# Optimization experiments

Measured on AMD Instinct MI355X. Metric: run time of the kernel, lower is better.

Reference implementation:

```python
import jax, jax.numpy as jnp
import numpy as np

EPS = 1e-5

def conv1x1(x, W, b):
    # x: (B,C,H,W), W: (O,C), b: (O,)
    return jnp.einsum('bchw,oc->bohw', x, W) + b[None, :, None, None]

def setup_inputs() -> dict:
    key = jax.random.key(0)
    ks = jax.random.split(key, 16)
    B, C_in, C1, D, K, H, Wd = 8, 512, 256, 128, 32, 96, 96
    s = lambda k, shape, fan: jax.random.normal(k, shape, jnp.float32) * (1.0 / np.sqrt(fan))
    return {
        'X': jax.random.normal(ks[0], (B, C_in, H, Wd), jnp.float32),
        'W_theta': s(ks[1], (C1, C_in), C_in), 'b_theta': jnp.zeros((C1,), jnp.float32),
        'W_phi': s(ks[2], (C1, C_in), C_in), 'b_phi': jnp.zeros((C1,), jnp.float32),
        'W_g': s(ks[3], (C1, C_in), C_in), 'b_g': jnp.zeros((C1,), jnp.float32),
        'W2': s(ks[4], (C_in, C1), C1), 'b2': jnp.zeros((C_in,), jnp.float32),
        'W3': s(ks[5], (D, C_in), C_in), 'b3': jnp.zeros((D,), jnp.float32),
        'codewords': jax.random.normal(ks[6], (K, D), jnp.float32),
        'scale': -jax.random.uniform(ks[7], (K,), jnp.float32),  # Deep-TEN init: U(-1,0)
        'W_fc': s(ks[8], (C_in, D), D), 'b_fc': jnp.zeros((C_in,), jnp.float32),
    }

def reference(X, W_theta, b_theta, W_phi, b_phi, W_g, b_g, W2, b2, W3, b3,
              codewords, scale, W_fc, b_fc):
    B, C_in, H, Wd = X.shape
    C1 = W_theta.shape[0]
    D, K = W3.shape[0], codewords.shape[0]
    N = H * Wd
    # --- non-local (channel-attention) block ---
    theta = conv1x1(X, W_theta, b_theta).reshape(B, C1, N)          # (B,C1,N)
    phi = conv1x1(X, W_phi, b_phi).reshape(B, C1, N)                # (B,C1,N)
    g = conv1x1(X, W_g, b_g).reshape(B, C1, N)                      # (B,C1,N)
    f = jax.nn.softmax(jnp.einsum('bcn,bdn->bcd', theta, phi), axis=-1)  # (B,C1,C1)
    y = jnp.einsum('bcd,bdn->bcn', f, g).reshape(B, C1, H, Wd)
    z = conv1x1(y, W2, b2) + X                                      # (B,C_in,H,W)
    # --- Deep-TEN encoding ---
    z_ = conv1x1(z, W3, b3)                                         # (B,D,H,W)
    x = z_.reshape(B, D, N).transpose(0, 2, 1)                      # (B,N,D)
    # squared L2 distances to codewords without (B,N,K,D) residuals
    dist = (jnp.sum(x * x, -1, keepdims=True)
            - 2.0 * jnp.einsum('bnd,kd->bnk', x, codewords)
            + jnp.sum(codewords * codewords, -1))                   # (B,N,K)
    A = jax.nn.softmax(scale * dist, axis=-1)                       # (B,N,K)
    # E_k = sum_i A_ik (x_i - c_k)
    E = jnp.einsum('bnk,bnd->bkd', A, x) - A.sum(1)[..., None] * codewords  # (B,K,D)
    # --- training-mode batch norm over K channels (no affine) ---
    mean = E.mean(axis=(0, 2), keepdims=True)
    var = E.var(axis=(0, 2), keepdims=True)
    e = jax.nn.relu((E - mean) * jax.lax.rsqrt(var + EPS))
    Es = e.sum(axis=1)                                              # (B,D)
    gamma = jax.nn.sigmoid(Es @ W_fc.T + b_fc)                      # (B,C_in)
    return z * gamma[:, :, None, None]
```

## Files before the change

kernel.cpp:

```cpp
#include <hip/hip_runtime.h>


typedef unsigned short u16;

#define Bb 8
#define Cc 512
#define C1 256
#define Dd 128
#define Kk 32
#define Nn 9216

typedef __attribute__((ext_vector_type(8))) short short8v;
typedef __attribute__((ext_vector_type(4))) short short4v;
typedef __attribute__((ext_vector_type(4))) float f32x4;

__device__ __forceinline__ float b2f(u16 u) {
  union { unsigned int i; float f; } v; v.i = ((unsigned int)u) << 16; return v.f;
}
__device__ __forceinline__ u16 f2b(float f) {
  union { float f; unsigned int i; } v; v.f = f;
  unsigned int x = v.i;
  return (u16)((x + 0x7fffu + ((x >> 16) & 1u)) >> 16);
}

__device__ __forceinline__ float b2fOrF(float x) { return x; }
__device__ __forceinline__ float b2fOrF(u16 x) { return b2f(x); }

__device__ __forceinline__ float4 load4(const float* p) { return *(const float4*)p; }
__device__ __forceinline__ float4 load4(const u16* p) {
  ushort4 q = *(const ushort4*)p;
  return make_float4(b2f(q.x), b2f(q.y), b2f(q.z), b2f(q.w));
}
__device__ __forceinline__ void store4(float* p, float a, float b, float c, float d) {
  *(float4*)p = make_float4(a, b, c, d);
}

__device__ __forceinline__ float waveSum(float v) {
  #pragma unroll
  for (int o = 32; o > 0; o >>= 1) v += __shfl_xor(v, o);
  return v;
}
__device__ __forceinline__ float waveMax(float v) {
  #pragma unroll
  for (int o = 32; o > 0; o >>= 1) v = fmaxf(v, __shfl_xor(v, o));
  return v;
}
__device__ __forceinline__ float blockSum256(float v) {
  __shared__ float sm[4];
  v = waveSum(v);
  if ((threadIdx.x & 63) == 0) sm[threadIdx.x >> 6] = v;
  __syncthreads();
  float r = sm[0] + sm[1] + sm[2] + sm[3];
  __syncthreads();
  return r;
}
__device__ __forceinline__ float blockMax256(float v) {
  __shared__ float sm[4];
  v = waveMax(v);
  if ((threadIdx.x & 63) == 0) sm[threadIdx.x >> 6] = v;
  __syncthreads();
  float r = fmaxf(fmaxf(sm[0], sm[1]), fmaxf(sm[2], sm[3]));
  __syncthreads();
  return r;
}

__device__ __forceinline__ f32x4 mfma_bf16_16x16x32(short8v a, short8v b, f32x4 c) {
  asm("v_mfma_f32_16x16x32_bf16 %0, %1, %2, %0" : "+v"(c) : "v"(a), "v"(b));
  return c;
}

__device__ __forceinline__ int fsw(int r) { return (r ^ (r >> 2) ^ (r >> 4)) & 3; }

__device__ __forceinline__ void cvt2(float x0, float x1, unsigned int& h, unsigned int& l) {
  asm("v_cvt_pk_bf16_f32 %0, %1, %2" : "=v"(h) : "v"(x0), "v"(x1));
  union { unsigned int u; float f; } fa, fb;
  fa.u = h << 16; fb.u = h & 0xffff0000u;
  float r0 = x0 - fa.f, r1 = x1 - fb.f;
  asm("v_cvt_pk_bf16_f32 %0, %1, %2" : "=v"(l) : "v"(r0), "v"(r1));
}

__device__ __forceinline__ void storeC(float* p, float v) { *p = v; }
__device__ __forceinline__ void storeC(u16* p, float v) { *p = f2b(v); }

template<typename TO, int NF>
__global__ __launch_bounds__(256, 2) void gemm_mfma(
    const float* __restrict__ A, const float* __restrict__ B, TO* __restrict__ C,
    int N, int K,
    long long sA, long long sB, long long sC,
    const float* __restrict__ biasRow, long long sBias,
    int gnx, int gny)
{
  static_assert(NF == 4 || NF == 8, "NF");
  constexpr int BN = 32 * NF;
  __shared__ __align__(16) u16 Asm_[2][128][40];
  __shared__ __align__(16) u16 Bsm_[2][BN][40];

  int id = blockIdx.x;
  {
    const int nwg = gridDim.x;
    if ((nwg & 7) == 0) id = (id & 7) * (nwg >> 3) + (id >> 3);
  }
  const int per = gnx * gny;
  const int b = id / per;
  const int rem = id - b * per;
  const int by = rem % gny;
  const int bx = rem / gny;
  A += b * sA; B += b * sB; C += b * sC;
  const int m0 = by * 128, n0 = bx * BN;

  const int t = threadIdx.x;
  const int w = t >> 6, lane = t & 63;
  const int wr = w >> 1, wc = w & 1;
  const int lr = lane & 15, lq = lane >> 4;

  const int sar = t >> 1, sak = (t & 1) * 16;
  const int kg = t >> 5, ng = t & 31;

  float ra[16];
  float rb[32];

  auto loadA = [&](int k0) {
    const float* p = A + (long long)(m0 + sar) * K + (k0 + sak);
    #pragma unroll
    for (int i = 0; i < 4; ++i) {
      float4 v = *(const float4*)(p + i * 4);
      ra[i*4+0] = v.x; ra[i*4+1] = v.y; ra[i*4+2] = v.z; ra[i*4+3] = v.w;
    }
  };
  auto loadB = [&](int k0) {
    const float* p = B + (long long)(k0 + kg * 4) * N + (n0 + ng * 8);
    #pragma unroll
    for (int i = 0; i < 4; ++i) {
      float4 v0 = *(const float4*)(p + (long long)i * N);
      float4 v1 = *(const float4*)(p + (long long)i * N + 4);
      rb[i*8+0]=v0.x; rb[i*8+1]=v0.y; rb[i*8+2]=v0.z; rb[i*8+3]=v0.w;
      rb[i*8+4]=v1.x; rb[i*8+5]=v1.y; rb[i*8+6]=v1.z; rb[i*8+7]=v1.w;
    }
  };

  auto stage = [&]() {
    {
      const int f = fsw(sar);
      #pragma unroll
      for (int h = 0; h < 2; ++h) {
        const int col = ((((sak >> 3) + h) ^ f) << 3);
        union { unsigned int u[4]; short8v v; } H, L;
        #pragma unroll
        for (int p = 0; p < 4; ++p) cvt2(ra[h*8+2*p], ra[h*8+2*p+1], H.u[p], L.u[p]);
        *(short8v*)&Asm_[0][sar][col] = H.v;
        *(short8v*)&Asm_[1][sar][col] = L.v;
      }
    }
    {
      #pragma unroll
      for (int j = 0; j < 8; ++j) {
        const int n = ng * 8 + j;
        const int col = (((kg >> 1) ^ fsw(n)) << 3) + (kg & 1) * 4;
        union { unsigned int u[2]; short4v v; } H, L;
        #pragma unroll
        for (int p = 0; p < 2; ++p)
          cvt2(rb[(2*p)*8 + j], rb[(2*p+1)*8 + j], H.u[p], L.u[p]);
        *(short4v*)&Bsm_[0][n][col] = H.v;
        *(short4v*)&Bsm_[1][n][col] = L.v;
      }
    }
  };

  f32x4 acc[4][NF];
  #pragma unroll
  for (int im = 0; im < 4; ++im)
    #pragma unroll
    for (int in = 0; in < NF; ++in)
      acc[im][in] = f32x4{0.f, 0.f, 0.f, 0.f};

  loadA(0); loadB(0);
  for (int k0 = 0; k0 < K; k0 += 32) {
    stage();
    if (k0 + 32 < K) { loadA(k0 + 32); loadB(k0 + 32); }
    __syncthreads();
    short8v af[2][4];
    #pragma unroll
    for (int im = 0; im < 4; ++im) {
      const int r = wr * 64 + im * 16 + lr;
      const int col = ((lq ^ fsw(r)) << 3);
      af[0][im] = *(const short8v*)&Asm_[0][r][col];
      af[1][im] = *(const short8v*)&Asm_[1][r][col];
    }
    #pragma unroll
    for (int in = 0; in < NF; ++in) {
      const int rB = wc * NF * 16 + in * 16 + lr;
      const int colB = ((lq ^ fsw(rB)) << 3);
      short8v bh = *(const short8v*)&Bsm_[0][rB][colB];
      short8v bl = *(const short8v*)&Bsm_[1][rB][colB];
      #pragma unroll
      for (int im = 0; im < 4; ++im) {
        acc[im][in] = mfma_bf16_16x16x32(af[0][im], bh, acc[im][in]);
        acc[im][in] = mfma_bf16_16x16x32(af[0][im], bl, acc[im][in]);
        acc[im][in] = mfma_bf16_16x16x32(af[1][im], bh, acc[im][in]);
      }
    }
    __syncthreads();
  }
  asm volatile("s_nop 7\n\ts_nop 7\n\ts_nop 7");

  #pragma unroll
  for (int im = 0; im < 4; ++im) {
    #pragma unroll
    for (int in = 0; in < NF; ++in) {
      const f32x4 a = acc[im][in];
      const int gc = n0 + wc * NF * 16 + in * 16 + lr;
      #pragma unroll
      for (int p = 0; p < 4; ++p) {
        const int gr = m0 + wr * 64 + im * 16 + lq * 4 + p;
        float v = a[p];
        if (biasRow) v += biasRow[b * sBias + gr];
        storeC(&C[(long long)gr * N + gc], v);
      }
    }
  }
}

__device__ __constant__ int PIa[10] = {0,0,0,0,1,1,1,2,2,3};
__device__ __constant__ int PJa[10] = {0,1,2,3,1,2,3,2,3,3};

__global__ __launch_bounds__(256, 2) void gxxt_kernel(
    const float* __restrict__ X, float* __restrict__ part,
    int numKS, int kChunk)
{
  __shared__ __align__(16) u16 Asm_[2][128][40];
  __shared__ __align__(16) u16 Bsm_[2][128][40];

  int id = blockIdx.x;
  {
    const int nwg = gridDim.x;
    if ((nwg & 7) == 0) id = (id & 7) * (nwg >> 3) + (id >> 3);
  }
  const int pair = id % 10;
  const int rest = id / 10;
  const int ks = rest % numKS;
  const int b = rest / numKS;
  const int i0 = PIa[pair] * 128, j0 = PJa[pair] * 128;
  const bool same = (i0 == j0);
  const float* Xb = X + (long long)b * Cc * Nn;
  const int kBeg = ks * kChunk, kEnd = kBeg + kChunk;

  const int t = threadIdx.x;
  const int w = t >> 6, lane = t & 63;
  const int wr = w >> 1, wc = w & 1;
  const int lr = lane & 15, lq = lane >> 4;
  const int sar = t >> 1, sak = (t & 1) * 16;

  float ra[16], rb[16];

  auto loadA = [&](int k0) {
    const float* p = Xb + (long long)(i0 + sar) * Nn + (k0 + sak);
    #pragma unroll
    for (int i = 0; i < 4; ++i) {
      float4 v = *(const float4*)(p + i * 4);
      ra[i*4+0] = v.x; ra[i*4+1] = v.y; ra[i*4+2] = v.z; ra[i*4+3] = v.w;
    }
  };
  auto loadB = [&](int k0) {
    const float* p = Xb + (long long)(j0 + sar) * Nn + (k0 + sak);
    #pragma unroll
    for (int i = 0; i < 4; ++i) {
      float4 v = *(const float4*)(p + i * 4);
      rb[i*4+0] = v.x; rb[i*4+1] = v.y; rb[i*4+2] = v.z; rb[i*4+3] = v.w;
    }
  };
  auto stageRow = [&](const float* s16, u16 (*H)[40], u16 (*L)[40]) {
    const int f = fsw(sar);
    #pragma unroll
    for (int h = 0; h < 2; ++h) {
      const int col = ((((sak >> 3) + h) ^ f) << 3);
      union { unsigned int u[4]; short8v v; } Hv, Lv;
      #pragma unroll
      for (int p = 0; p < 4; ++p) cvt2(s16[h*8+2*p], s16[h*8+2*p+1], Hv.u[p], Lv.u[p]);
      *(short8v*)&H[sar][col] = Hv.v;
      *(short8v*)&L[sar][col] = Lv.v;
    }
  };

  const u16 (*BH)[40] = same ? Asm_[0] : Bsm_[0];
  const u16 (*BL)[40] = same ? Asm_[1] : Bsm_[1];

  f32x4 acc[4][4];
  #pragma unroll
  for (int im = 0; im < 4; ++im)
    #pragma unroll
    for (int in = 0; in < 4; ++in)
      acc[im][in] = f32x4{0.f, 0.f, 0.f, 0.f};

  loadA(kBeg);
  if (!same) loadB(kBeg);
  for (int k0 = kBeg; k0 < kEnd; k0 += 32) {
    stageRow(ra, Asm_[0], Asm_[1]);
    if (!same) stageRow(rb, Bsm_[0], Bsm_[1]);
    if (k0 + 32 < kEnd) { loadA(k0 + 32); if (!same) loadB(k0 + 32); }
    __syncthreads();
    short8v af[2][4];
    #pragma unroll
    for (int im = 0; im < 4; ++im) {
      const int r = wr * 64 + im * 16 + lr;
      const int col = ((lq ^ fsw(r)) << 3);
      af[0][im] = *(const short8v*)&Asm_[0][r][col];
      af[1][im] = *(const short8v*)&Asm_[1][r][col];
    }
    #pragma unroll
    for (int in = 0; in < 4; ++in) {
      const int rB = wc * 64 + in * 16 + lr;
      const int colB = ((lq ^ fsw(rB)) << 3);
      short8v bh = *(const short8v*)&BH[rB][colB];
      short8v bl = *(const short8v*)&BL[rB][colB];
      #pragma unroll
      for (int im = 0; im < 4; ++im) {
        acc[im][in] = mfma_bf16_16x16x32(af[0][im], bh, acc[im][in]);
        acc[im][in] = mfma_bf16_16x16x32(af[0][im], bl, acc[im][in]);
        acc[im][in] = mfma_bf16_16x16x32(af[1][im], bh, acc[im][in]);
      }
    }
    __syncthreads();
  }
  asm volatile("s_nop 7\n\ts_nop 7\n\ts_nop 7");

  float* Cp = part + ((long long)(ks * Bb + b) * 10 + pair) * 16384;
  #pragma unroll
  for (int im = 0; im < 4; ++im) {
    #pragma unroll
    for (int in = 0; in < 4; ++in) {
      const f32x4 a = acc[im][in];
      const int gc = wc * 64 + in * 16 + lr;
      #pragma unroll
      for (int p = 0; p < 4; ++p) {
        const int gr = wr * 64 + im * 16 + lq * 4 + p;
        Cp[gr * 128 + gc] = a[p];
      }
    }
  }
}

__global__ __launch_bounds__(256) void gred_kernel(const float* __restrict__ part,
    float* __restrict__ G, int numKS) {
  __shared__ float sm[64][129];
  const int pair = blockIdx.x % 10, b = blockIdx.x / 10;
  const int i0 = PIa[pair] * 128, j0 = PJa[pair] * 128;
  float* Gb = G + (long long)b * Cc * Cc;
  const long long ksStr = (long long)Bb * 10 * 16384;
  const float* p0 = part + ((long long)b * 10 + pair) * 16384;
  const int t = threadIdx.x;
  for (int half = 0; half < 2; ++half) {
    const int r0 = half * 64;
    __syncthreads();
    for (int rep = 0; rep < 32; ++rep) {
      int idx = r0 * 128 + rep * 256 + t;
      float s = 0.f;
      for (int ks = 0; ks < numKS; ++ks) s += p0[(long long)ks * ksStr + idx];
      int r = (idx >> 7) - r0, c = idx & 127;
      sm[r][c] = s;
      Gb[(long long)(i0 + r0 + r) * Cc + (j0 + c)] = s;
    }
    if (i0 != j0) {
      __syncthreads();
      for (int rep = 0; rep < 32; ++rep) {
        int o = rep * 256 + t;
        int rr = o >> 6, cc = o & 63;
        Gb[(long long)(j0 + rr) * Cc + (i0 + r0 + cc)] = sm[cc][rr];
      }
    }
  }
}

template<bool TRANSB>
__global__ __launch_bounds__(256) void gemm64(
    const float* __restrict__ A, const float* __restrict__ B, float* __restrict__ C,
    int M, int N, int K,
    long long sA, long long sB, long long sC,
    const float* __restrict__ biasRow, long long sBias)
{
  const int bz = blockIdx.z;
  A += (long long)bz * sA;
  B += (long long)bz * sB;
  C += (long long)bz * sC;
  const int m0 = blockIdx.y * 64, n0 = blockIdx.x * 64;
  __shared__ __align__(16) float As[16][64];
  __shared__ __align__(16) float Bs[16][64];
  const int t = threadIdx.x;
  const int lr = t >> 2, lk = (t & 3) << 2;
  const int tm = (t >> 4) << 2, tn = (t & 15) << 2;
  float acc[4][4] = {};
  for (int k0 = 0; k0 < K; k0 += 16) {
    {
      float4 a = load4(A + (long long)(m0 + lr) * K + (k0 + lk));
      As[lk + 0][lr] = a.x; As[lk + 1][lr] = a.y; As[lk + 2][lr] = a.z; As[lk + 3][lr] = a.w;
    }
    if (TRANSB) {
      float4 b = load4(B + (long long)(n0 + lr) * K + (k0 + lk));
      Bs[lk + 0][lr] = b.x; Bs[lk + 1][lr] = b.y; Bs[lk + 2][lr] = b.z; Bs[lk + 3][lr] = b.w;
    } else {
      const int kr = t >> 4, nc = (t & 15) << 2;
      float4 b = load4(B + (long long)(k0 + kr) * N + (n0 + nc));
      *(float4*)&Bs[kr][nc] = b;
    }
    __syncthreads();
    #pragma unroll
    for (int kk = 0; kk < 16; ++kk) {
      const float4 av = *(const float4*)&As[kk][tm];
      const float4 bv = *(const float4*)&Bs[kk][tn];
      acc[0][0] = fmaf(av.x, bv.x, acc[0][0]);
      acc[0][1] = fmaf(av.x, bv.y, acc[0][1]);
      acc[0][2] = fmaf(av.x, bv.z, acc[0][2]);
      acc[0][3] = fmaf(av.x, bv.w, acc[0][3]);
      acc[1][0] = fmaf(av.y, bv.x, acc[1][0]);
      acc[1][1] = fmaf(av.y, bv.y, acc[1][1]);
      acc[1][2] = fmaf(av.y, bv.z, acc[1][2]);
      acc[1][3] = fmaf(av.y, bv.w, acc[1][3]);
      acc[2][0] = fmaf(av.z, bv.x, acc[2][0]);
      acc[2][1] = fmaf(av.z, bv.y, acc[2][1]);
      acc[2][2] = fmaf(av.z, bv.z, acc[2][2]);
      acc[2][3] = fmaf(av.z, bv.w, acc[2][3]);
      acc[3][0] = fmaf(av.w, bv.x, acc[3][0]);
      acc[3][1] = fmaf(av.w, bv.y, acc[3][1]);
      acc[3][2] = fmaf(av.w, bv.z, acc[3][2]);
      acc[3][3] = fmaf(av.w, bv.w, acc[3][3]);
    }
    __syncthreads();
  }
  #pragma unroll
  for (int i = 0; i < 4; ++i) {
    const int m = m0 + tm + i;
    float bias = biasRow ? biasRow[bz * sBias + m] : 0.f;
    store4(C + (long long)m * N + (n0 + tn),
           acc[i][0] + bias, acc[i][1] + bias, acc[i][2] + bias, acc[i][3] + bias);
  }
}

__global__ __launch_bounds__(256) void rowsum_kernel(const float* __restrict__ X,
                                                     float* __restrict__ s, int N) {
  long long row = blockIdx.x;
  const float* p = X + row * N;
  float acc = 0.f;
  for (int i = threadIdx.x; i < N; i += 256) acc += p[i];
  acc = blockSum256(acc);
  if (threadIdx.x == 0) s[row] = acc;
}

__global__ __launch_bounds__(256) void gemv512_kernel(const float* __restrict__ W,
                                                      const float* __restrict__ s,
                                                      float* __restrict__ out) {
  int b = blockIdx.x;
  __shared__ float ssm[Cc];
  for (int i = threadIdx.x; i < Cc; i += 256) ssm[i] = s[b * Cc + i];
  __syncthreads();
  int i = threadIdx.x;
  const float* wr = W + i * Cc;
  float acc = 0.f;
  for (int k = 0; k < Cc; ++k) acc = fmaf(wr[k], ssm[k], acc);
  out[b * C1 + i] = acc;
}

__global__ __launch_bounds__(256) void softmax_kernel(float* __restrict__ L,
    const float* __restrict__ bth, const float* __restrict__ bph,
    const float* __restrict__ u, const float* __restrict__ v) {
  int row = blockIdx.x;
  int b = row >> 8, i = row & 255;
  int j = threadIdx.x;
  float bt = bth[i], bp = bph[j];
  long long idx = (long long)row * C1 + j;
  float val = L[idx] + bt * v[b * C1 + j] + u[b * C1 + i] * bp + (float)Nn * bt * bp;
  float mx = blockMax256(val);
  float p = expf(val - mx);
  float sm = blockSum256(p);
  L[idx] = p / sm;
}

__global__ __launch_bounds__(256) void w_kernel(const float* __restrict__ f,
                                                const float* __restrict__ bg,
                                                float* __restrict__ w) {
  int b = blockIdx.x;
  __shared__ float bgs[C1];
  bgs[threadIdx.x] = bg[threadIdx.x];
  __syncthreads();
  int i = threadIdx.x;
  const float* fr = f + ((long long)b * C1 + i) * C1;
  float acc = 0.f;
  for (int j = 0; j < C1; ++j) acc = fmaf(fr[j], bgs[j], acc);
  w[b * C1 + i] = acc;
}

__global__ __launch_bounds__(256) void q_kernel(const float* __restrict__ W2,
                                                const float* __restrict__ b2v,
                                                const float* __restrict__ w,
                                                float* __restrict__ q) {
  int gi = blockIdx.x * 256 + threadIdx.x;
  int b = gi >> 9, c = gi & 511;
  __shared__ float wsm[C1];
  wsm[threadIdx.x] = w[b * C1 + threadIdx.x];
  __syncthreads();
  const float* wr = W2 + c * C1;
  float acc = b2v[c];
  for (int i = 0; i < C1; ++i) acc = fmaf(wr[i], wsm[i], acc);
  q[gi] = acc;
}

__global__ __launch_bounds__(256) void adddiag_kernel(float* __restrict__ P) {
  int gi = blockIdx.x * 256 + threadIdx.x;
  int b = gi >> 9, c = gi & 511;
  P[((long long)b * Cc + c) * Cc + c] += 1.f;
}

__global__ __launch_bounds__(256) void zqbias_kernel(const float* __restrict__ W3,
    const float* __restrict__ b3, const float* __restrict__ q, float* __restrict__ zqb) {
  int gi = blockIdx.x * 256 + threadIdx.x;
  int b = gi >> 7, d = gi & 127;
  const float* wr = W3 + d * Cc;
  const float* qr = q + b * Cc;
  float acc = b3[d];
  for (int c = 0; c < Cc; ++c) acc = fmaf(wr[c], qr[c], acc);
  zqb[gi] = acc;
}

template<typename ZT>
__global__ __launch_bounds__(256) void enc_kernel(
    const ZT* __restrict__ zq,
    const float* __restrict__ cw,
    const float* __restrict__ sc,
    float* __restrict__ Eraw,
    float* __restrict__ Asum)
{
  __shared__ float csm[Kk][Dd + 1];
  __shared__ float cc[Kk], ssm[Kk];
  __shared__ float sA[Kk][256 + 1];
  __shared__ float zs[Dd][17];
  const int tid = threadIdx.x;
  const int b = blockIdx.y;
  const int n0 = blockIdx.x * 256;

  #pragma unroll
  for (int r = 0; r < 16; ++r) {
    int idx = r * 256 + tid;
    csm[idx >> 7][idx & 127] = cw[idx];
  }
  if (tid < Kk) ssm[tid] = sc[tid];
  __syncthreads();
  if (tid < Kk) {
    float a = 0.f;
    for (int d = 0; d < Dd; ++d) { float cv = csm[tid][d]; a = fmaf(cv, cv, a); }
    cc[tid] = a;
  }
  __syncthreads();

  const int n = n0 + tid;
  const ZT* zp = zq + (long long)b * Dd * Nn + n;
  float dots[Kk];
  #pragma unroll
  for (int k = 0; k < Kk; ++k) dots[k] = 0.f;
  float xx = 0.f;
  for (int d = 0; d < Dd; ++d) {
    float xv = b2fOrF(zp[(long long)d * Nn]);
    xx = fmaf(xv, xv, xx);
    #pragma unroll
    for (int k = 0; k < Kk; ++k) dots[k] = fmaf(csm[k][d], xv, dots[k]);
  }
  float mx = -1e30f;
  #pragma unroll
  for (int k = 0; k < Kk; ++k) {
    float l = ssm[k] * (xx - 2.f * dots[k] + cc[k]);
    dots[k] = l;
    mx = fmaxf(mx, l);
  }
  float sum = 0.f;
  #pragma unroll
  for (int k = 0; k < Kk; ++k) { float p = expf(dots[k] - mx); dots[k] = p; sum += p; }
  float inv = 1.f / sum;
  #pragma unroll
  for (int k = 0; k < Kk; ++k) sA[k][tid] = dots[k] * inv;
  __syncthreads();
  if (tid < Kk) {
    float s = 0.f;
    for (int p = 0; p < 256; ++p) s += sA[tid][p];
    atomicAdd(&Asum[b * Kk + tid], s);
  }

  float acc[16];
  #pragma unroll
  for (int j = 0; j < 16; ++j) acc[j] = 0.f;
  const int k = tid & 31, d0 = (tid >> 5) * 16;
  const int ldd = tid >> 1, lpx = (tid & 1) * 8;
  for (int it = 0; it < 16; ++it) {
    __syncthreads();
    {
      const ZT* src = zq + ((long long)b * Dd + ldd) * Nn + n0 + it * 16 + lpx;
      float4 a4 = load4(src);
      float4 b4 = load4(src + 4);
      zs[ldd][lpx + 0] = a4.x; zs[ldd][lpx + 1] = a4.y;
      zs[ldd][lpx + 2] = a4.z; zs[ldd][lpx + 3] = a4.w;
      zs[ldd][lpx + 4] = b4.x; zs[ldd][lpx + 5] = b4.y;
      zs[ldd][lpx + 6] = b4.z; zs[ldd][lpx + 7] = b4.w;
    }
    __syncthreads();
    #pragma unroll
    for (int p = 0; p < 16; ++p) {
      float a = sA[k][it * 16 + p];
      #pragma unroll
      for (int j = 0; j < 16; ++j) acc[j] = fmaf(a, zs[d0 + j][p], acc[j]);
    }
  }
  float* Ep = Eraw + ((long long)b * Kk + k) * Dd + d0;
  #pragma unroll
  for (int j = 0; j < 16; ++j) atomicAdd(Ep + j, acc[j]);
}

__global__ __launch_bounds__(256) void bn_kernel(const float* __restrict__ Eraw,
    const float* __restrict__ Asum, const float* __restrict__ cw, float* __restrict__ Es) {
  int k = blockIdx.x, tid = threadIdx.x;
  float vals[4], s = 0.f, s2 = 0.f;
  #pragma unroll
  for (int r = 0; r < 4; ++r) {
    int i = r * 256 + tid;
    int b = i >> 7, d = i & 127;
    float e = Eraw[((long long)b * Kk + k) * Dd + d] - Asum[b * Kk + k] * cw[k * Dd + d];
    vals[r] = e; s += e; s2 = fmaf(e, e, s2);
  }
  s = blockSum256(s);
  s2 = blockSum256(s2);
  float mean = s * (1.f / 1024.f);
  float var = fmaxf(s2 * (1.f / 1024.f) - mean * mean, 0.f);
  float rs = rsqrtf(var + 1e-5f);
  #pragma unroll
  for (int r = 0; r < 4; ++r) {
    int i = r * 256 + tid;
    int b = i >> 7, d = i & 127;
    float e = (vals[r] - mean) * rs;
    if (e > 0.f) atomicAdd(&Es[b * Dd + d], e);
  }
}

__global__ __launch_bounds__(256) void gamma_kernel(const float* __restrict__ Es,
    const float* __restrict__ Wfc, const float* __restrict__ bfc, float* __restrict__ gam) {
  int gi = blockIdx.x * 256 + threadIdx.x;
  int b = gi >> 9, c = gi & 511;
  __shared__ float esm[Dd];
  if (threadIdx.x < Dd) esm[threadIdx.x] = Es[b * Dd + threadIdx.x];
  __syncthreads();
  const float* wr = Wfc + c * Dd;
  float acc = bfc[c];
  for (int d = 0; d < Dd; ++d) acc = fmaf(wr[d], esm[d], acc);
  gam[gi] = 1.f / (1.f + expf(-acc));
}

__global__ __launch_bounds__(256) void scaleout_f32(float* __restrict__ out,
    const float* __restrict__ gam) {
  unsigned int idx = blockIdx.x * 256u + threadIdx.x;
  unsigned int f = idx * 4u;
  unsigned int bc = f / (unsigned)Nn;
  float g = gam[bc];
  float4 zv = *(const float4*)(out + f);
  store4(out + f, zv.x * g, zv.y * g, zv.z * g, zv.w * g);
}

extern "C" void kernel_launch(void* const* d_in, const int* in_sizes, int n_in,
                              void* d_out, int out_size, void* d_ws, size_t ws_size,
                              hipStream_t stream) {
  const float* X   = (const float*)d_in[0];
  const float* Wth = (const float*)d_in[1];
  const float* bth = (const float*)d_in[2];
  const float* Wph = (const float*)d_in[3];
  const float* bph = (const float*)d_in[4];
  const float* Wg  = (const float*)d_in[5];
  const float* bg  = (const float*)d_in[6];
  const float* W2  = (const float*)d_in[7];
  const float* b2v = (const float*)d_in[8];
  const float* W3  = (const float*)d_in[9];
  const float* b3v = (const float*)d_in[10];
  const float* CW  = (const float*)d_in[11];
  const float* SC  = (const float*)d_in[12];
  const float* Wfc = (const float*)d_in[13];
  const float* bfc = (const float*)d_in[14];
  float* out = (float*)d_out;
  float* wsf = (float*)d_ws;

  const long long szL   = (long long)Bb * C1 * C1;
  const long long szRA  = (long long)Bb * Cc * Cc;
  const long long szRB  = (long long)Bb * C1 * Cc;
  long long off = 0;
  float* s_   = wsf + off; off += Bb * Cc;
  float* u_   = wsf + off; off += Bb * C1;
  float* v_   = wsf + off; off += Bb * C1;
  float* w_   = wsf + off; off += Bb * C1;
  float* q_   = wsf + off; off += Bb * Cc;
  float* Eraw_= wsf + off; off += (long long)Bb * Kk * Dd;
  float* Es_  = wsf + off; off += Bb * Dd;
  float* Asum_= wsf + off; off += Bb * Kk;
  float* gam_ = wsf + off; off += Bb * Cc;
  float* L_   = wsf + off; off += szL;
  float* regA = wsf + off; off += szRA;
  float* regB = wsf + off; off += szRB;
  const long long baseFloats = off;
  float* tail = wsf + off;
  const long long ZQ_F  = (long long)Bb * Dd * Nn;
  const long long tailFloats = (long long)(ws_size / 4) - baseFloats;
  const bool big = tailFloats >= ZQ_F;
  const int numKS = big ? 6 : 2;
  float* part = tail;
  float* zqf  = tail;
  u16*   zqh  = (u16*)tail;
  float* R_   = L_;
  float* zqb_ = u_;

  const long long strX = (long long)Cc * Nn;
  const long long sG = (long long)Cc * Cc;
  const long long sU = (long long)C1 * Cc;
  const long long sL = (long long)C1 * C1;
  const long long sR = (long long)Dd * Cc;

  rowsum_kernel<<<Bb * Cc, 256, 0, stream>>>(X, s_, Nn);
  gxxt_kernel<<<dim3(10 * numKS * Bb), 256, 0, stream>>>(X, part, numKS, Nn / numKS);
  gred_kernel<<<dim3(10 * Bb), 256, 0, stream>>>(part, regA, numKS);
  gemm64<false><<<dim3(8, 4, Bb), 256, 0, stream>>>(
      Wth, regA, regB, C1, Cc, Cc, 0, sG, sU, nullptr, 0);
  gemv512_kernel<<<Bb, 256, 0, stream>>>(Wth, s_, u_);
  gemv512_kernel<<<Bb, 256, 0, stream>>>(Wph, s_, v_);
  gemm64<true><<<dim3(4, 4, Bb), 256, 0, stream>>>(
      regB, Wph, L_, C1, C1, Cc, sU, 0, sL, nullptr, 0);
  softmax_kernel<<<Bb * C1, 256, 0, stream>>>(L_, bth, bph, u_, v_);
  w_kernel<<<Bb, 256, 0, stream>>>(L_, bg, w_);
  gemm64<false><<<dim3(8, 4, Bb), 256, 0, stream>>>(
      L_, Wg, regB, C1, Cc, C1, sL, 0, sU, nullptr, 0);
  q_kernel<<<16, 256, 0, stream>>>(W2, b2v, w_, q_);
  gemm64<false><<<dim3(8, 8, Bb), 256, 0, stream>>>(
      W2, regB, regA, Cc, Cc, C1, 0, sU, sG, nullptr, 0);
  adddiag_kernel<<<16, 256, 0, stream>>>(regA);
  gemm64<false><<<dim3(8, 2, Bb), 256, 0, stream>>>(
      W3, regA, R_, Dd, Cc, Cc, 0, sG, sR, nullptr, 0);
  zqbias_kernel<<<4, 256, 0, stream>>>(W3, b3v, q_, zqb_);
  gemm_mfma<float, 8><<<dim3(1152), 256, 0, stream>>>(
      regA, X, out, Nn, Cc, sG, strX, strX, q_, Cc, 36, 4);
  hipMemsetAsync(Eraw_, 0, (size_t)(Bb * Kk * Dd + Bb * Dd + Bb * Kk) * 4, stream);
  if (big) {
    gemm_mfma<float, 8><<<dim3(288), 256, 0, stream>>>(
        R_, X, zqf, Nn, Cc, sR, strX, (long long)Dd * Nn, zqb_, Dd, 36, 1);
    enc_kernel<float><<<dim3(36, Bb), 256, 0, stream>>>(zqf, CW, SC, Eraw_, Asum_);
  } else {
    gemm_mfma<u16, 8><<<dim3(288), 256, 0, stream>>>(
        R_, X, zqh, Nn, Cc, sR, strX, (long long)Dd * Nn, zqb_, Dd, 36, 1);
    enc_kernel<u16><<<dim3(36, Bb), 256, 0, stream>>>(zqh, CW, SC, Eraw_, Asum_);
  }
  bn_kernel<<<Kk, 256, 0, stream>>>(Eraw_, Asum_, CW, Es_);
  gamma_kernel<<<16, 256, 0, stream>>>(Es_, Wfc, bfc, gam_);
  const unsigned int n4 = (unsigned)(Bb * Cc * Nn / 4);
  scaleout_f32<<<n4 / 256, 256, 0, stream>>>(out, gam_);
  (void)in_sizes; (void)n_in; (void)out_size;
}
```

Measured before the change: 1.099 ms.

## Fuse gamma scaling into output GEMM, transpose zq layout, move small GEMMs to MFMA

The big output GEMM now runs after gamma is computed and multiplies by gamma in its epilogue. This removes the separate full-tensor read-modify-write pass over the output. The zq GEMM now writes pixel-major (N,D) with vector stores, and enc_kernel reads contiguous rows and transposed shared tiles instead of strided columns. The small channel GEMMs switch from gemm64 to the MFMA kernel, which launches few blocks and may underuse the device.

Measured after the change: 1.096 ms. No clear change (-0.3%).

```diff
diff --git a/kernel.cpp b/kernel.cpp
--- a/kernel.cpp
+++ b/kernel.cpp
@@ -23,9 +23,6 @@
   return (u16)((x + 0x7fffu + ((x >> 16) & 1u)) >> 16);
 }
 
-__device__ __forceinline__ float b2fOrF(float x) { return x; }
-__device__ __forceinline__ float b2fOrF(u16 x) { return b2f(x); }
-
 __device__ __forceinline__ float4 load4(const float* p) { return *(const float4*)p; }
 __device__ __forceinline__ float4 load4(const u16* p) {
   ushort4 q = *(const ushort4*)p;
@@ -79,18 +76,22 @@
   asm("v_cvt_pk_bf16_f32 %0, %1, %2" : "=v"(l) : "v"(r0), "v"(r1));
 }
 
-__device__ __forceinline__ void storeC(float* p, float v) { *p = v; }
-__device__ __forceinline__ void storeC(u16* p, float v) { *p = f2b(v); }
-
-template<typename TO, int NF>
+__device__ __forceinline__ void storeC4(float* p, float4 v) { *(float4*)p = v; }
+__device__ __forceinline__ void storeC4(u16* p, float4 v) {
+  ushort4 q; q.x = f2b(v.x); q.y = f2b(v.y); q.z = f2b(v.z); q.w = f2b(v.w);
+  *(ushort4*)p = q;
+}
+
+template<typename TO, int NF, int OMODE>
 __global__ __launch_bounds__(256, 2) void gemm_mfma(
     const float* __restrict__ A, const float* __restrict__ B, TO* __restrict__ C,
     int N, int K,
     long long sA, long long sB, long long sC,
     const float* __restrict__ biasRow, long long sBias,
+    const float* __restrict__ scaleRow,
     int gnx, int gny)
 {
-  static_assert(NF == 4 || NF == 8, "NF");
+  static_assert(NF == 8, "NF");
   constexpr int BN = 32 * NF;
   __shared__ __align__(16) u16 Asm_[2][128][40];
   __shared__ __align__(16) u16 Bsm_[2][BN][40];
@@ -203,18 +204,35 @@
   }
   asm volatile("s_nop 7\n\ts_nop 7\n\ts_nop 7");
 
-  #pragma unroll
-  for (int im = 0; im < 4; ++im) {
-    #pragma unroll
-    for (int in = 0; in < NF; ++in) {
-      const f32x4 a = acc[im][in];
-      const int gc = n0 + wc * NF * 16 + in * 16 + lr;
-      #pragma unroll
-      for (int p = 0; p < 4; ++p) {
-        const int gr = m0 + wr * 64 + im * 16 + lq * 4 + p;
-        float v = a[p];
-        if (biasRow) v += biasRow[b * sBias + gr];
-        storeC(&C[(long long)gr * N + gc], v);
+  if constexpr (OMODE == 1) {
+    const float* bb = biasRow + (long long)b * sBias;
+    #pragma unroll
+    for (int im = 0; im < 4; ++im) {
+      #pragma unroll
+      for (int in = 0; in < NF; ++in) {
+        const f32x4 a = acc[im][in];
+        const int gc = n0 + wc * NF * 16 + in * 16 + lr;
+        const int d0b = wr * 64 + im * 16 + lq * 4;
+        float4 v = make_float4(a[0] + bb[d0b + 0], a[1] + bb[d0b + 1],
+                               a[2] + bb[d0b + 2], a[3] + bb[d0b + 3]);
+        storeC4(&C[(long long)gc * Dd + d0b], v);
+      }
+    }
+  } else {
+    #pragma unroll
+    for (int im = 0; im < 4; ++im) {
+      #pragma unroll
+      for (int in = 0; in < NF; ++in) {
+        const f32x4 a = acc[im][in];
+        const int gc = n0 + wc * NF * 16 + in * 16 + lr;
+        #pragma unroll
+        for (int p = 0; p < 4; ++p) {
+          const int gr = m0 + wr * 64 + im * 16 + lq * 4 + p;
+          float v = a[p];
+          if (biasRow) v += biasRow[b * sBias + gr];
+          if (scaleRow) v *= scaleRow[b * sBias + gr];
+          C[(long long)gr * N + gc] = v;
+        }
       }
     }
   }
@@ -530,7 +548,7 @@
   __shared__ float csm[Kk][Dd + 1];
   __shared__ float cc[Kk], ssm[Kk];
   __shared__ float sA[Kk][256 + 1];
-  __shared__ float zs[Dd][17];
+  __shared__ float zs[16][Dd + 4];
   const int tid = threadIdx.x;
   const int b = blockIdx.y;
   const int n0 = blockIdx.x * 256;
@@ -549,17 +567,24 @@
   }
   __syncthreads();
 
-  const int n = n0 + tid;
-  const ZT* zp = zq + (long long)b * Dd * Nn + n;
+  const ZT* zrow = zq + ((long long)b * Nn + n0 + tid) * Dd;
   float dots[Kk];
   #pragma unroll
   for (int k = 0; k < Kk; ++k) dots[k] = 0.f;
   float xx = 0.f;
-  for (int d = 0; d < Dd; ++d) {
-    float xv = b2fOrF(zp[(long long)d * Nn]);
-    xx = fmaf(xv, xv, xx);
-    #pragma unroll
-    for (int k = 0; k < Kk; ++k) dots[k] = fmaf(csm[k][d], xv, dots[k]);
+  for (int d = 0; d < Dd; d += 4) {
+    float4 xv = load4(zrow + d);
+    xx = fmaf(xv.x, xv.x, xx); xx = fmaf(xv.y, xv.y, xx);
+    xx = fmaf(xv.z, xv.z, xx); xx = fmaf(xv.w, xv.w, xx);
+    #pragma unroll
+    for (int k = 0; k < Kk; ++k) {
+      float dk = dots[k];
+      dk = fmaf(csm[k][d + 0], xv.x, dk);
+      dk = fmaf(csm[k][d + 1], xv.y, dk);
+      dk = fmaf(csm[k][d + 2], xv.z, dk);
+      dk = fmaf(csm[k][d + 3], xv.w, dk);
+      dots[k] = dk;
+    }
   }
   float mx = -1e30f;
   #pragma unroll
@@ -585,24 +610,22 @@
   #pragma unroll
   for (int j = 0; j < 16; ++j) acc[j] = 0.f;
   const int k = tid & 31, d0 = (tid >> 5) * 16;
-  const int ldd = tid >> 1, lpx = (tid & 1) * 8;
+  const int spx = tid >> 4, sd = (tid & 15) * 8;
   for (int it = 0; it < 16; ++it) {
     __syncthreads();
     {
-      const ZT* src = zq + ((long long)b * Dd + ldd) * Nn + n0 + it * 16 + lpx;
+      const ZT* src = zq + ((long long)b * Nn + n0 + it * 16 + spx) * Dd + sd;
       float4 a4 = load4(src);
       float4 b4 = load4(src + 4);
-      zs[ldd][lpx + 0] = a4.x; zs[ldd][lpx + 1] = a4.y;
-      zs[ldd][lpx + 2] = a4.z; zs[ldd][lpx + 3] = a4.w;
-      zs[ldd][lpx + 4] = b4.x; zs[ldd][lpx + 5] = b4.y;
-      zs[ldd][lpx + 6] = b4.z; zs[ldd][lpx + 7] = b4.w;
+      *(float4*)&zs[spx][sd] = a4;
+      *(float4*)&zs[spx][sd + 4] = b4;
     }
     __syncthreads();
     #pragma unroll
     for (int p = 0; p < 16; ++p) {
       float a = sA[k][it * 16 + p];
       #pragma unroll
-      for (int j = 0; j < 16; ++j) acc[j] = fmaf(a, zs[d0 + j][p], acc[j]);
+      for (int j = 0; j < 16; ++j) acc[j] = fmaf(a, zs[p][d0 + j], acc[j]);
     }
   }
   float* Ep = Eraw + ((long long)b * Kk + k) * Dd + d0;
@@ -646,16 +669,6 @@
   float acc = bfc[c];
   for (int d = 0; d < Dd; ++d) acc = fmaf(wr[d], esm[d], acc);
   gam[gi] = 1.f / (1.f + expf(-acc));
-}
-
-__global__ __launch_bounds__(256) void scaleout_f32(float* __restrict__ out,
-    const float* __restrict__ gam) {
-  unsigned int idx = blockIdx.x * 256u + threadIdx.x;
-  unsigned int f = idx * 4u;
-  unsigned int bc = f / (unsigned)Nn;
-  float g = gam[bc];
-  float4 zv = *(const float4*)(out + f);
-  store4(out + f, zv.x * g, zv.y * g, zv.z * g, zv.w * g);
 }
 
 extern "C" void kernel_launch(void* const* d_in, const int* in_sizes, int n_in,
@@ -716,38 +729,36 @@
   rowsum_kernel<<<Bb * Cc, 256, 0, stream>>>(X, s_, Nn);
   gxxt_kernel<<<dim3(10 * numKS * Bb), 256, 0, stream>>>(X, part, numKS, Nn / numKS);
   gred_kernel<<<dim3(10 * Bb), 256, 0, stream>>>(part, regA, numKS);
-  gemm64<false><<<dim3(8, 4, Bb), 256, 0, stream>>>(
-      Wth, regA, regB, C1, Cc, Cc, 0, sG, sU, nullptr, 0);
+  gemm_mfma<float, 8, 0><<<dim3(32), 256, 0, stream>>>(
+      Wth, regA, regB, Cc, Cc, 0, sG, sU, nullptr, 0, nullptr, 2, 2);
   gemv512_kernel<<<Bb, 256, 0, stream>>>(Wth, s_, u_);
   gemv512_kernel<<<Bb, 256, 0, stream>>>(Wph, s_, v_);
   gemm64<true><<<dim3(4, 4, Bb), 256, 0, stream>>>(
       regB, Wph, L_, C1, C1, Cc, sU, 0, sL, nullptr, 0);
   softmax_kernel<<<Bb * C1, 256, 0, stream>>>(L_, bth, bph, u_, v_);
   w_kernel<<<Bb, 256, 0, stream>>>(L_, bg, w_);
-  gemm64<false><<<dim3(8, 4, Bb), 256, 0, stream>>>(
-      L_, Wg, regB, C1, Cc, C1, sL, 0, sU, nullptr, 0);
+  gemm_mfma<float, 8, 0><<<dim3(32), 256, 0, stream>>>(
+      L_, Wg, regB, Cc, C1, sL, 0, sU, nullptr, 0, nullptr, 2, 2);
   q_kernel<<<16, 256, 0, stream>>>(W2, b2v, w_, q_);
-  gemm64<false><<<dim3(8, 8, Bb), 256, 0, stream>>>(
-      W2, regB, regA, Cc, Cc, C1, 0, sU, sG, nullptr, 0);
+  gemm_mfma<float, 8, 0><<<dim3(64), 256, 0, stream>>>(
+      W2, regB, regA, Cc, C1, 0, sU, sG, nullptr, 0, nullptr, 2, 4);
   adddiag_kernel<<<16, 256, 0, stream>>>(regA);
-  gemm64<false><<<dim3(8, 2, Bb), 256, 0, stream>>>(
-      W3, regA, R_, Dd, Cc, Cc, 0, sG, sR, nullptr, 0);
+  gemm_mfma<float, 8, 0><<<dim3(16), 256, 0, stream>>>(
+      W3, regA, R_, Cc, Cc, 0, sG, sR, nullptr, 0, nullptr, 2, 1);
   zqbias_kernel<<<4, 256, 0, stream>>>(W3, b3v, q_, zqb_);
-  gemm_mfma<float, 8><<<dim3(1152), 256, 0, stream>>>(
-      regA, X, out, Nn, Cc, sG, strX, strX, q_, Cc, 36, 4);
   hipMemsetAsync(Eraw_, 0, (size_t)(Bb * Kk * Dd + Bb * Dd + Bb * Kk) * 4, stream);
   if (big) {
-    gemm_mfma<float, 8><<<dim3(288), 256, 0, stream>>>(
-        R_, X, zqf, Nn, Cc, sR, strX, (long long)Dd * Nn, zqb_, Dd, 36, 1);
+    gemm_mfma<float, 8, 1><<<dim3(288), 256, 0, stream>>>(
+        R_, X, zqf, Nn, Cc, sR, strX, (long long)Dd * Nn, zqb_, Dd, nullptr, 36, 1);
     enc_kernel<float><<<dim3(36, Bb), 256, 0, stream>>>(zqf, CW, SC, Eraw_, Asum_);
   } else {
-    gemm_mfma<u16, 8><<<dim3(288), 256, 0, stream>>>(
-        R_, X, zqh, Nn, Cc, sR, strX, (long long)Dd * Nn, zqb_, Dd, 36, 1);
+    gemm_mfma<u16, 8, 1><<<dim3(288), 256, 0, stream>>>(
+        R_, X, zqh, Nn, Cc, sR, strX, (long long)Dd * Nn, zqb_, Dd, nullptr, 36, 1);
     enc_kernel<u16><<<dim3(36, Bb), 256, 0, stream>>>(zqh, CW, SC, Eraw_, Asum_);
   }
   bn_kernel<<<Kk, 256, 0, stream>>>(Eraw_, Asum_, CW, Es_);
   gamma_kernel<<<16, 256, 0, stream>>>(Es_, Wfc, bfc, gam_);
-  const unsigned int n4 = (unsigned)(Bb * Cc * Nn / 4);
-  scaleout_f32<<<n4 / 256, 256, 0, stream>>>(out, gam_);
+  gemm_mfma<float, 8, 0><<<dim3(1152), 256, 0, stream>>>(
+      regA, X, out, Nn, Cc, sG, strX, strX, q_, Cc, gam_, 36, 4);
   (void)in_sizes; (void)n_in; (void)out_size;
 }
```
